# Performance work log

Hardware: AMD Instinct MI355X
Metric: run time of the kernel (lower is better)

## Reference

```python
import jax, jax.numpy as jnp
import numpy as np

N, C, D = 16384, 1000, 1024

def setup_inputs() -> dict:
    key = jax.random.key(0)
    k1, k2 = jax.random.split(key)
    embedding = jax.random.normal(k1, (N, D), dtype=jnp.float32)
    # nn.Parameter init is zeros in the module, but zeros give degenerate (all-equal)
    # distances; use random centers as a trained-parameter stand-in.
    centers = jax.random.normal(k2, (C, D), dtype=jnp.float32)
    return {"embedding": embedding, "centers": centers}

def reference(embedding, centers):
    # pytorch_ood.utils.pairwise_distances: squared Euclidean via norm + matmul trick
    x_norm = jnp.sum(embedding * embedding, axis=1, keepdims=True)      # [N, 1]
    y_norm = jnp.sum(centers * centers, axis=1)[None, :]                # [1, C]
    dist = x_norm + y_norm - 2.0 * jnp.matmul(embedding, centers.T)     # [N, C]
    return jnp.maximum(dist, 0.0)
```

## Files before the change

### kernel.cpp

```cpp
#include <hip/hip_runtime.h>
#include <hip/hip_bf16.h>
#include <stdint.h>

#define N_ROWS 16384
#define C_ROWS 1000
#define C_PAD  1024
#define D_DIM  1024

#define KSTEPS 32
#define TILE_ELEMS 4096
#define KT 16

typedef __attribute__((ext_vector_type(8))) short    bf16x8;
typedef __attribute__((ext_vector_type(4))) float    f32x4;
typedef __attribute__((ext_vector_type(4))) uint32_t u32x4;

__device__ __forceinline__ uint32_t pk2bf(float lo, float hi) {
    union { float f; uint32_t u; } a, b;
    a.f = lo; b.f = hi;
    uint32_t l = (a.u + 0x8000u) >> 16;
    uint32_t h = (b.u + 0x8000u) >> 16;
    return l | (h << 16);
}

__device__ __forceinline__ void gl_lds16(const uint16_t* g, uint16_t* l) {
    __builtin_amdgcn_global_load_lds(
        (const __attribute__((address_space(1))) void*)g,
        (__attribute__((address_space(3))) void*)l,
        16, 0, 0);
}

__global__ void convert_norm_tiled(const float* __restrict__ x,
                                   uint16_t* __restrict__ xt,
                                   float* __restrict__ norms,
                                   int rows, int pad_rows) {
    int wid  = (blockIdx.x * blockDim.x + threadIdx.x) >> 6;
    int lane = threadIdx.x & 63;
    if (wid >= pad_rows) return;
    const int tile = wid >> 7;
    const int row  = wid & 127;
    uint16_t* tbase = xt + (size_t)tile * KSTEPS * TILE_ELEMS;
    const int kslot = lane & 3;
    const int cellb = (kslot * 128 + row) * 8;
    if (wid < rows) {
        const f32x4* rp = (const f32x4*)(x + (size_t)wid * D_DIM);
        float s = 0.f;
#pragma unroll
        for (int i = 0; i < 2; ++i) {
            f32x4 v0 = rp[i * 128 + lane * 2];
            f32x4 v1 = rp[i * 128 + lane * 2 + 1];
            s += v0[0]*v0[0] + v0[1]*v0[1] + v0[2]*v0[2] + v0[3]*v0[3]
               + v1[0]*v1[0] + v1[1]*v1[1] + v1[2]*v1[2] + v1[3]*v1[3];
            u32x4 p;
            p[0] = pk2bf(v0[0], v0[1]); p[1] = pk2bf(v0[2], v0[3]);
            p[2] = pk2bf(v1[0], v1[1]); p[3] = pk2bf(v1[2], v1[3]);
            const int t = i * 16 + (lane >> 2);
            *(u32x4*)(tbase + (size_t)t * TILE_ELEMS + cellb) = p;
        }
#pragma unroll
        for (int off = 32; off > 0; off >>= 1) s += __shfl_down(s, off, 64);
        if (lane == 0) norms[wid] = s;
    } else {
        u32x4 z = {0, 0, 0, 0};
#pragma unroll
        for (int i = 0; i < 2; ++i) {
            const int t = i * 16 + (lane >> 2);
            *(u32x4*)(tbase + (size_t)t * TILE_ELEMS + cellb) = z;
        }
        if (lane == 0) norms[wid] = 0.f;
    }
}

__global__ __launch_bounds__(512, 2)
void dist_gemm3(const uint16_t* __restrict__ At,
                const uint16_t* __restrict__ Bt,
                const float* __restrict__ xn,
                const float* __restrict__ yn,
                float* __restrict__ out) {
    __shared__ uint16_t As[2][4 * TILE_ELEMS];
    __shared__ uint16_t Bs[2][4 * TILE_ELEMS];

    const int tid  = threadIdx.x;
    const int lane = tid & 63;
    const int wid  = tid >> 6;
    const int wm   = wid >> 2;
    const int wn   = wid & 3;

    const int R  = blockIdx.x;
    const int Cc = blockIdx.y;

    const uint16_t* A0 = At + (size_t)(2 * R)      * KSTEPS * TILE_ELEMS;
    const uint16_t* A1 = A0 + (size_t)KSTEPS * TILE_ELEMS;
    const uint16_t* B0 = Bt + (size_t)(2 * Cc)     * KSTEPS * TILE_ELEMS;
    const uint16_t* B1 = B0 + (size_t)KSTEPS * TILE_ELEMS;
    const int so = tid * 8;

    const int fA = ((lane >> 4) * 128 + (lane & 15)) * 8;
    const int fB = ((lane >> 4) * 128 + (wn & 1) * 64 + (lane & 15)) * 8;
    const int aslot = wm * 2;
    const int bslot = (wn >> 1) * 2;

    f32x4 acc[8][4];
#pragma unroll
    for (int m = 0; m < 8; ++m)
#pragma unroll
        for (int n = 0; n < 4; ++n) acc[m][n] = (f32x4)(0.f);

#define STAGE3(buf, t)                                                        \
    do {                                                                      \
        size_t g = (size_t)(2 * (t)) * TILE_ELEMS;                            \
        gl_lds16(A0 + g + so,              &As[buf][0 * TILE_ELEMS + so]);    \
        gl_lds16(A0 + g + TILE_ELEMS + so, &As[buf][1 * TILE_ELEMS + so]);    \
        gl_lds16(A1 + g + so,              &As[buf][2 * TILE_ELEMS + so]);    \
        gl_lds16(A1 + g + TILE_ELEMS + so, &As[buf][3 * TILE_ELEMS + so]);    \
        gl_lds16(B0 + g + so,              &Bs[buf][0 * TILE_ELEMS + so]);    \
        gl_lds16(B0 + g + TILE_ELEMS + so, &Bs[buf][1 * TILE_ELEMS + so]);    \
        gl_lds16(B1 + g + so,              &Bs[buf][2 * TILE_ELEMS + so]);    \
        gl_lds16(B1 + g + TILE_ELEMS + so, &Bs[buf][3 * TILE_ELEMS + so]);    \
    } while (0)

    STAGE3(0, 0);
    __syncthreads();

    int cur = 0;
    for (int t = 0; t < KT; ++t) {
        if (t + 1 < KT) STAGE3(cur ^ 1, t + 1);
#pragma unroll
        for (int kk = 0; kk < 2; ++kk) {
            const uint16_t* Ab = &As[cur][(aslot + kk) * TILE_ELEMS];
            const uint16_t* Bb = &Bs[cur][(bslot + kk) * TILE_ELEMS];
            bf16x8 a[8], b[4];
#pragma unroll
            for (int m = 0; m < 8; ++m) a[m] = *(const bf16x8*)(Ab + fA + m * 128);
#pragma unroll
            for (int n = 0; n < 4; ++n) b[n] = *(const bf16x8*)(Bb + fB + n * 128);
#pragma unroll
            for (int m = 0; m < 8; ++m)
#pragma unroll
                for (int n = 0; n < 4; ++n)
                    acc[m][n] = __builtin_amdgcn_mfma_f32_16x16x32_bf16(
                        a[m], b[n], acc[m][n], 0, 0, 0);
        }
        __syncthreads();
        cur ^= 1;
    }
#undef STAGE3

    const int orow0 = R * 256 + wm * 128 + ((lane >> 4) * 4);
    const int ocol0 = Cc * 256 + wn * 64 + (lane & 15);
#pragma unroll
    for (int n = 0; n < 4; ++n) {
        int gc = ocol0 + n * 16;
        if (gc >= C_ROWS) continue;
        float ynv = yn[gc];
#pragma unroll
        for (int m = 0; m < 8; ++m) {
            int gr = orow0 + m * 16;
#pragma unroll
            for (int r = 0; r < 4; ++r) {
                float v = xn[gr + r] + ynv - 2.0f * acc[m][n][r];
                out[(size_t)(gr + r) * C_ROWS + gc] = fmaxf(v, 0.f);
            }
        }
    }
}

__global__ void row_norms_kernel(const float* __restrict__ x,
                                 float* __restrict__ out,
                                 int rows, int pad_rows) {
    int gid  = blockIdx.x * blockDim.x + threadIdx.x;
    int wid  = gid >> 6;
    int lane = threadIdx.x & 63;
    if (wid >= pad_rows) return;
    float s = 0.f;
    if (wid < rows) {
        const f32x4* rp = (const f32x4*)(x + (size_t)wid * D_DIM);
#pragma unroll
        for (int r = 0; r < D_DIM / 256; ++r) {
            f32x4 v = rp[r * 64 + lane];
            s += v[0]*v[0] + v[1]*v[1] + v[2]*v[2] + v[3]*v[3];
        }
    }
#pragma unroll
    for (int off = 32; off > 0; off >>= 1) s += __shfl_down(s, off, 64);
    if (lane == 0) out[wid] = s;
}

__global__ __launch_bounds__(256, 2)
void dist_gemm_kernel(const float* __restrict__ E,
                      const float* __restrict__ Cc,
                      const float* __restrict__ xn,
                      const float* __restrict__ yn,
                      float* __restrict__ out) {
    __shared__ uint16_t As[4 * 128 * 8];
    __shared__ uint16_t Bs[4 * 128 * 8];
    const int tid  = threadIdx.x;
    const int lane = tid & 63;
    const int wid  = tid >> 6;
    const int wm   = wid >> 1;
    const int wn   = wid & 1;
    const int rowTile = blockIdx.y;
    const int colTile = blockIdx.x;
    const int srow = tid & 127;
    const int sp   = tid >> 7;
    const int ga = rowTile * 128 + srow;
    const int gb = colTile * 128 + srow;
    const float* Arow = E  + (size_t)ga * D_DIM + sp * 16;
    const float* Brow = Cc + (size_t)gb * D_DIM + sp * 16;
    const bool bvalid = (gb < C_ROWS);
    f32x4 acc[4][4];
#pragma unroll
    for (int m = 0; m < 4; ++m)
#pragma unroll
        for (int n = 0; n < 4; ++n) acc[m][n] = (f32x4)(0.f);
    const int fragA_base = (((lane >> 4) * 128) + wm * 64 + (lane & 15)) * 8;
    const int fragB_base = (((lane >> 4) * 128) + wn * 64 + (lane & 15)) * 8;
    const int stA0 = ((sp * 2) * 128 + srow) * 8;
    const int stA1 = ((sp * 2 + 1) * 128 + srow) * 8;
    for (int k0 = 0; k0 < D_DIM; k0 += 32) {
        f32x4 a0 = *(const f32x4*)(Arow + k0);
        f32x4 a1 = *(const f32x4*)(Arow + k0 + 4);
        f32x4 a2 = *(const f32x4*)(Arow + k0 + 8);
        f32x4 a3 = *(const f32x4*)(Arow + k0 + 12);
        f32x4 b0 = (f32x4)(0.f), b1 = (f32x4)(0.f),
              b2 = (f32x4)(0.f), b3 = (f32x4)(0.f);
        if (bvalid) {
            b0 = *(const f32x4*)(Brow + k0);
            b1 = *(const f32x4*)(Brow + k0 + 4);
            b2 = *(const f32x4*)(Brow + k0 + 8);
            b3 = *(const f32x4*)(Brow + k0 + 12);
        }
        u32x4 pa01, pa23, pb01, pb23;
        pa01[0] = pk2bf(a0[0], a0[1]); pa01[1] = pk2bf(a0[2], a0[3]);
        pa01[2] = pk2bf(a1[0], a1[1]); pa01[3] = pk2bf(a1[2], a1[3]);
        pa23[0] = pk2bf(a2[0], a2[1]); pa23[1] = pk2bf(a2[2], a2[3]);
        pa23[2] = pk2bf(a3[0], a3[1]); pa23[3] = pk2bf(a3[2], a3[3]);
        pb01[0] = pk2bf(b0[0], b0[1]); pb01[1] = pk2bf(b0[2], b0[3]);
        pb01[2] = pk2bf(b1[0], b1[1]); pb01[3] = pk2bf(b1[2], b1[3]);
        pb23[0] = pk2bf(b2[0], b2[1]); pb23[1] = pk2bf(b2[2], b2[3]);
        pb23[2] = pk2bf(b3[0], b3[1]); pb23[3] = pk2bf(b3[2], b3[3]);
        __syncthreads();
        *(u32x4*)&As[stA0] = pa01;
        *(u32x4*)&As[stA1] = pa23;
        *(u32x4*)&Bs[stA0] = pb01;
        *(u32x4*)&Bs[stA1] = pb23;
        __syncthreads();
        bf16x8 ar[4], br[4];
#pragma unroll
        for (int m = 0; m < 4; ++m) ar[m] = *(const bf16x8*)&As[fragA_base + m * 16 * 8];
#pragma unroll
        for (int n = 0; n < 4; ++n) br[n] = *(const bf16x8*)&Bs[fragB_base + n * 16 * 8];
#pragma unroll
        for (int m = 0; m < 4; ++m)
#pragma unroll
            for (int n = 0; n < 4; ++n)
                acc[m][n] = __builtin_amdgcn_mfma_f32_16x16x32_bf16(
                    ar[m], br[n], acc[m][n], 0, 0, 0);
    }
    const int orow0 = rowTile * 128 + wm * 64 + ((lane >> 4) * 4);
    const int ocol0 = colTile * 128 + wn * 64 + (lane & 15);
#pragma unroll
    for (int n = 0; n < 4; ++n) {
        int gc = ocol0 + n * 16;
        if (gc >= C_ROWS) continue;
        float ynv = yn[gc];
#pragma unroll
        for (int m = 0; m < 4; ++m) {
            int gr = orow0 + m * 16;
#pragma unroll
            for (int r = 0; r < 4; ++r) {
                float v = xn[gr + r] + ynv - 2.0f * acc[m][n][r];
                out[(size_t)(gr + r) * C_ROWS + gc] = fmaxf(v, 0.f);
            }
        }
    }
}

extern "C" void kernel_launch(void* const* d_in, const int* in_sizes, int n_in,
                              void* d_out, int out_size, void* d_ws, size_t ws_size,
                              hipStream_t stream) {
    const float* E  = (const float*)d_in[0];
    const float* Cc = (const float*)d_in[1];
    float* out = (float*)d_out;

    uint16_t* Et = (uint16_t*)d_ws;
    uint16_t* Ct = Et + (size_t)N_ROWS * D_DIM;
    float*    xn = (float*)(Ct + (size_t)C_PAD * D_DIM);
    float*    yn = xn + N_ROWS;
    size_t need = (size_t)((char*)(yn + C_PAD) - (char*)d_ws);

    if (ws_size >= need) {
        convert_norm_tiled<<<N_ROWS / 4, 256, 0, stream>>>(E,  Et, xn, N_ROWS, N_ROWS);
        convert_norm_tiled<<<C_PAD  / 4, 256, 0, stream>>>(Cc, Ct, yn, C_ROWS, C_PAD);
        dim3 grid(N_ROWS / 256, C_PAD / 256);
        dist_gemm3<<<grid, 512, 0, stream>>>(Et, Ct, xn, yn, out);
    } else {
        float* fxn = (float*)d_ws;
        float* fyn = fxn + N_ROWS;
        row_norms_kernel<<<N_ROWS / 4, 256, 0, stream>>>(E,  fxn, N_ROWS, N_ROWS);
        row_norms_kernel<<<C_PAD  / 4, 256, 0, stream>>>(Cc, fyn, C_ROWS, C_PAD);
        dim3 grid(C_PAD / 128, N_ROWS / 128);
        dist_gemm_kernel<<<grid, 256, 0, stream>>>(E, Cc, fxn, fyn, out);
    }
}
```

Before: 76.89 us.

## Restructure GEMM main loop into 4-stage half-tile pipeline with fine-grained waits

Replaces the double-buffered full-K-tile loop with a four-slot ring of half-size LDS buffers. Global-to-LDS loads are issued in interleaved A and B pieces between MFMA groups, paced by explicit vmcnt waits and raw s_barrier instead of __syncthreads. MFMA sections are wrapped in s_setprio so they are favoured over other waves. The aim is to hide memory latency more evenly and cut register pressure by loading only half of the A fragments at a time, at the cost of more barriers and hand-tuned waitcnt values that must match the issue order exactly.

```diff
diff --git a/kernel.cpp b/kernel.cpp
--- a/kernel.cpp
+++ b/kernel.cpp
@@ -71,14 +71,35 @@
     }
 }
 
+__device__ __forceinline__ void rdA(bf16x8 (&a)[4], const uint16_t* base,
+                                    int fA, int mh) {
+#pragma unroll
+    for (int i = 0; i < 4; ++i)
+        a[i] = *(const bf16x8*)(base + fA + (mh * 4 + i) * 128);
+}
+__device__ __forceinline__ void rdB(bf16x8 (&b)[4], const uint16_t* base, int fB) {
+#pragma unroll
+    for (int n = 0; n < 4; ++n)
+        b[n] = *(const bf16x8*)(base + fB + n * 128);
+}
+__device__ __forceinline__ void mfma16(f32x4 (&acc)[8][4], int mh,
+                                       const bf16x8 (&a)[4], const bf16x8 (&b)[4]) {
+#pragma unroll
+    for (int i = 0; i < 4; ++i)
+#pragma unroll
+        for (int n = 0; n < 4; ++n)
+            acc[mh * 4 + i][n] = __builtin_amdgcn_mfma_f32_16x16x32_bf16(
+                a[i], b[n], acc[mh * 4 + i][n], 0, 0, 0);
+}
+
 __global__ __launch_bounds__(512, 2)
-void dist_gemm3(const uint16_t* __restrict__ At,
+void dist_gemm4(const uint16_t* __restrict__ At,
                 const uint16_t* __restrict__ Bt,
                 const float* __restrict__ xn,
                 const float* __restrict__ yn,
                 float* __restrict__ out) {
-    __shared__ uint16_t As[2][4 * TILE_ELEMS];
-    __shared__ uint16_t Bs[2][4 * TILE_ELEMS];
+    __shared__ uint16_t Ah[4][2 * TILE_ELEMS];
+    __shared__ uint16_t Bh[4][2 * TILE_ELEMS];
 
     const int tid  = threadIdx.x;
     const int lane = tid & 63;
@@ -89,16 +110,16 @@
     const int R  = blockIdx.x;
     const int Cc = blockIdx.y;
 
-    const uint16_t* A0 = At + (size_t)(2 * R)      * KSTEPS * TILE_ELEMS;
+    const uint16_t* A0 = At + (size_t)(2 * R)  * KSTEPS * TILE_ELEMS;
     const uint16_t* A1 = A0 + (size_t)KSTEPS * TILE_ELEMS;
-    const uint16_t* B0 = Bt + (size_t)(2 * Cc)     * KSTEPS * TILE_ELEMS;
+    const uint16_t* B0 = Bt + (size_t)(2 * Cc) * KSTEPS * TILE_ELEMS;
     const uint16_t* B1 = B0 + (size_t)KSTEPS * TILE_ELEMS;
     const int so = tid * 8;
 
-    const int fA = ((lane >> 4) * 128 + (lane & 15)) * 8;
-    const int fB = ((lane >> 4) * 128 + (wn & 1) * 64 + (lane & 15)) * 8;
-    const int aslot = wm * 2;
-    const int bslot = (wn >> 1) * 2;
+    const int fA   = ((lane >> 4) * 128 + (lane & 15)) * 8;
+    const int fB   = ((lane >> 4) * 128 + (wn & 1) * 64 + (lane & 15)) * 8;
+    const int aoff = wm * TILE_ELEMS;
+    const int boff = (wn >> 1) * TILE_ELEMS;
 
     f32x4 acc[8][4];
 #pragma unroll
@@ -106,45 +127,59 @@
 #pragma unroll
         for (int n = 0; n < 4; ++n) acc[m][n] = (f32x4)(0.f);
 
-#define STAGE3(buf, t)                                                        \
-    do {                                                                      \
-        size_t g = (size_t)(2 * (t)) * TILE_ELEMS;                            \
-        gl_lds16(A0 + g + so,              &As[buf][0 * TILE_ELEMS + so]);    \
-        gl_lds16(A0 + g + TILE_ELEMS + so, &As[buf][1 * TILE_ELEMS + so]);    \
-        gl_lds16(A1 + g + so,              &As[buf][2 * TILE_ELEMS + so]);    \
-        gl_lds16(A1 + g + TILE_ELEMS + so, &As[buf][3 * TILE_ELEMS + so]);    \
-        gl_lds16(B0 + g + so,              &Bs[buf][0 * TILE_ELEMS + so]);    \
-        gl_lds16(B0 + g + TILE_ELEMS + so, &Bs[buf][1 * TILE_ELEMS + so]);    \
-        gl_lds16(B1 + g + so,              &Bs[buf][2 * TILE_ELEMS + so]);    \
-        gl_lds16(B1 + g + TILE_ELEMS + so, &Bs[buf][3 * TILE_ELEMS + so]);    \
+    bf16x8 a_[4], b_[4];
+
+#define ISSA(s, q) do { \
+        gl_lds16(A0 + (size_t)(q) * TILE_ELEMS + so, &Ah[s][so]); \
+        gl_lds16(A1 + (size_t)(q) * TILE_ELEMS + so, &Ah[s][TILE_ELEMS + so]); } while (0)
+#define ISSB(s, q) do { \
+        gl_lds16(B0 + (size_t)(q) * TILE_ELEMS + so, &Bh[s][so]); \
+        gl_lds16(B1 + (size_t)(q) * TILE_ELEMS + so, &Bh[s][TILE_ELEMS + so]); } while (0)
+
+#define TILE_BODY(s0, s1, sn0, sn1, q0, q1, PREF, VMA, VMB)                    \
+    do {                                                                       \
+        if (PREF) ISSA(sn0, q0);                                               \
+        asm volatile("s_waitcnt vmcnt(" VMA ")" ::: "memory");                 \
+        __builtin_amdgcn_s_barrier();                                          \
+        asm volatile("" ::: "memory");                                         \
+        rdA(a_, &Ah[s0][aoff], fA, 0); rdB(b_, &Bh[s0][boff], fB);             \
+        __builtin_amdgcn_s_setprio(1); mfma16(acc, 0, a_, b_);                 \
+        __builtin_amdgcn_s_setprio(0);                                         \
+        __builtin_amdgcn_s_barrier();                                          \
+        if (PREF) ISSB(sn0, q0);                                               \
+        rdA(a_, &Ah[s0][aoff], fA, 1);                                         \
+        __builtin_amdgcn_s_setprio(1); mfma16(acc, 1, a_, b_);                 \
+        __builtin_amdgcn_s_setprio(0);                                         \
+        __builtin_amdgcn_s_barrier();                                          \
+        if (PREF) ISSA(sn1, q1);                                               \
+        asm volatile("s_waitcnt vmcnt(" VMB ")" ::: "memory");                 \
+        __builtin_amdgcn_s_barrier();                                          \
+        asm volatile("" ::: "memory");                                         \
+        rdA(a_, &Ah[s1][aoff], fA, 0); rdB(b_, &Bh[s1][boff], fB);             \
+        __builtin_amdgcn_s_setprio(1); mfma16(acc, 0, a_, b_);                 \
+        __builtin_amdgcn_s_setprio(0);                                         \
+        __builtin_amdgcn_s_barrier();                                          \
+        if (PREF) ISSB(sn1, q1);                                               \
+        rdA(a_, &Ah[s1][aoff], fA, 1);                                         \
+        __builtin_amdgcn_s_setprio(1); mfma16(acc, 1, a_, b_);                 \
+        __builtin_amdgcn_s_setprio(0);                                         \
+        __builtin_amdgcn_s_barrier();                                          \
     } while (0)
 
-    STAGE3(0, 0);
-    __syncthreads();
-
-    int cur = 0;
-    for (int t = 0; t < KT; ++t) {
-        if (t + 1 < KT) STAGE3(cur ^ 1, t + 1);
-#pragma unroll
-        for (int kk = 0; kk < 2; ++kk) {
-            const uint16_t* Ab = &As[cur][(aslot + kk) * TILE_ELEMS];
-            const uint16_t* Bb = &Bs[cur][(bslot + kk) * TILE_ELEMS];
-            bf16x8 a[8], b[4];
-#pragma unroll
-            for (int m = 0; m < 8; ++m) a[m] = *(const bf16x8*)(Ab + fA + m * 128);
-#pragma unroll
-            for (int n = 0; n < 4; ++n) b[n] = *(const bf16x8*)(Bb + fB + n * 128);
-#pragma unroll
-            for (int m = 0; m < 8; ++m)
-#pragma unroll
-                for (int n = 0; n < 4; ++n)
-                    acc[m][n] = __builtin_amdgcn_mfma_f32_16x16x32_bf16(
-                        a[m], b[n], acc[m][n], 0, 0, 0);
-        }
-        __syncthreads();
-        cur ^= 1;
-    }
-#undef STAGE3
+    ISSA(0, 0); ISSB(0, 0); ISSA(1, 1); ISSB(1, 1);
+
+#pragma unroll 1
+    for (int tt = 0; tt < 7; ++tt) {
+        const int t0 = 2 * tt;
+        TILE_BODY(0, 1, 2, 3, 2 * t0 + 2, 2 * t0 + 3, true, "6", "6");
+        TILE_BODY(2, 3, 0, 1, 2 * t0 + 4, 2 * t0 + 5, true, "6", "6");
+    }
+    TILE_BODY(0, 1, 2, 3, 30, 31, true, "6", "6");
+    TILE_BODY(2, 3, 0, 1, 0, 0, false, "4", "0");
+
+#undef TILE_BODY
+#undef ISSA
+#undef ISSB
 
     const int orow0 = R * 256 + wm * 128 + ((lane >> 4) * 4);
     const int ocol0 = Cc * 256 + wn * 64 + (lane & 15);
@@ -293,7 +328,7 @@
         convert_norm_tiled<<<N_ROWS / 4, 256, 0, stream>>>(E,  Et, xn, N_ROWS, N_ROWS);
         convert_norm_tiled<<<C_PAD  / 4, 256, 0, stream>>>(Cc, Ct, yn, C_ROWS, C_PAD);
         dim3 grid(N_ROWS / 256, C_PAD / 256);
-        dist_gemm3<<<grid, 512, 0, stream>>>(Et, Ct, xn, yn, out);
+        dist_gemm4<<<grid, 512, 0, stream>>>(Et, Ct, xn, yn, out);
     } else {
         float* fxn = (float*)d_ws;
         float* fyn = fxn + N_ROWS;
```

Measured after the change: 70.92 us. 1.08x faster.
